# Kernel optimization log

Measured on AMD Instinct MI355X. Metric: run time of the kernel, lower is better.

## Reference

```python
import jax, jax.numpy as jnp
import numpy as np

LR = 0.01
DECAY = 0.9


def setup_inputs() -> dict:
    key = jax.random.key(0)
    ks = jax.random.split(key, 8)
    B, D_IN, H, N_FLUX, N_MET, N_IN, N_REF = 32768, 128, 1024, 512, 256, 128, 64
    return {
        "input": jax.random.normal(ks[0], (B, D_IN), jnp.float32),
        "Vref": jax.random.normal(ks[1], (B, N_REF), jnp.float32),
        "Vin": jax.random.normal(ks[2], (B, N_IN), jnp.float32),
        "W1": jax.random.normal(ks[3], (D_IN, H), jnp.float32) * 0.02,
        "b1": jnp.zeros((H,), jnp.float32),
        "W2": jax.random.normal(ks[4], (H, N_FLUX), jnp.float32) * 0.02,
        "b2": jnp.zeros((N_FLUX,), jnp.float32),
        "S": jax.random.normal(ks[5], (N_MET, N_FLUX), jnp.float32) * 0.1,
        "Pin": jax.random.normal(ks[6], (N_IN, N_FLUX), jnp.float32) * 0.1,
        "n_iteration": 30,
    }


def reference(input, Vref, Vin, W1, b1, W2, b2, S, Pin, n_iteration):
    # MLP head: Linear -> ReLU -> (Dropout inactive at eval) -> Linear
    V0 = jnp.maximum(input @ W1 + b1, 0.0) @ W2 + b2  # [B, n_flux]
    n_met = S.shape[0]
    n_in = Pin.shape[0]
    n_flux = V0.shape[1]

    def step(carry, _):
        V, diff = carry
        # dL2/dV = 2/n_met * (V S^T) S
        dV2 = (V @ S.T) @ S * (2.0 / n_met)
        # dL3/dV = 2/n_in * relu(V Pin^T - Vin) Pin  (indicator*relu == relu)
        relu_vin = jnp.maximum(V @ Pin.T - Vin, 0.0)
        dV3 = relu_vin @ Pin * (2.0 / n_in)
        # dL4/dV = -2/n_flux * relu(-V) = 2/n_flux * min(V, 0)
        dV4 = jnp.minimum(V, 0.0) * (2.0 / n_flux)
        dV = dV2 + dV3 + dV4
        diff_new = DECAY * diff - LR * dV
        return (V + diff_new, diff_new), None

    (V, _), _ = jax.lax.scan(step, (V0, jnp.zeros_like(V0)), None, length=n_iteration)
    return V
```

## Files before the change

kernel.cpp:

```cpp
#include <hip/hip_runtime.h>

typedef __bf16 bhalf;
typedef __bf16 bh8_t __attribute__((ext_vector_type(8)));
typedef float f4_t __attribute__((ext_vector_type(4)));

#define MFMA16(A, B, C) __builtin_amdgcn_mfma_f32_16x16x32_bf16((A), (B), (C), 0, 0, 0)


#define OFF_W1T  0
#define OFF_W2T  (OFF_W1T + 1024 * 128)
#define OFF_PINB (OFF_W2T + 512 * 1024)
#define OFF_PT   (OFF_PINB + 128 * 512)
#define OFF_G    (OFF_PT + 512 * 128)

__global__ __launch_bounds__(256) void amn_prep(
    const float* __restrict__ W1, const float* __restrict__ W2,
    const float* __restrict__ Pin, bhalf* __restrict__ ws) {
  unsigned i = blockIdx.x * 256u + threadIdx.x;
  if (i < 131072u) {
    unsigned n = i >> 7, k = i & 127u;
    ws[OFF_W1T + i] = (bhalf)W1[k * 1024u + n];
  } else if (i < 655360u) {
    unsigned j = i - 131072u;
    unsigned n = j >> 10, k = j & 1023u;
    ws[OFF_W2T + j] = (bhalf)W2[k * 512u + n];
  } else if (i < 720896u) {
    unsigned j = i - 655360u;
    ws[OFF_PINB + j] = (bhalf)Pin[j];
  } else if (i < 786432u) {
    unsigned j = i - 720896u;
    unsigned n = j >> 7, k = j & 127u;
    ws[OFF_PT + j] = (bhalf)(Pin[k * 512u + n] * 0.015625f);
  }
}

__global__ __launch_bounds__(256) void amn_gram(
    const float* __restrict__ S, bhalf* __restrict__ ws) {
  const unsigned bi = blockIdx.x >> 5, bj = blockIdx.x & 31u;
  __shared__ float SA[256][16];
  __shared__ float SB[256][16];
  const unsigned t = threadIdx.x;
#pragma unroll
  for (int p = 0; p < 16; ++p) {
    unsigned e = p * 256u + t;
    unsigned k = e >> 4, c = e & 15u;
    SA[k][c] = S[k * 512u + bi * 16u + c];
    SB[k][c] = S[k * 512u + bj * 16u + c];
  }
  __syncthreads();
  const unsigned ti = t >> 4, tj = t & 15u;
  float acc = 0.f;
#pragma unroll 8
  for (int k = 0; k < 256; ++k) acc += SA[k][ti] * SB[k][tj];
  ws[OFF_G + (bi * 16u + ti) * 512u + bj * 16u + tj] = (bhalf)(acc * 0.0078125f);
}

__device__ inline bh8_t cvt8(f4_t f0, f4_t f1) {
  bh8_t r;
  r[0] = (bhalf)f0[0]; r[1] = (bhalf)f0[1]; r[2] = (bhalf)f0[2]; r[3] = (bhalf)f0[3];
  r[4] = (bhalf)f1[0]; r[5] = (bhalf)f1[1]; r[6] = (bhalf)f1[2]; r[7] = (bhalf)f1[3];
  return r;
}
__device__ inline unsigned pk2(float a, float b) {
  union { bhalf h; unsigned short s; } x, y;
  x.h = (bhalf)a; y.h = (bhalf)b;
  return (unsigned)x.s | ((unsigned)y.s << 16);
}
__device__ inline float up_lo(unsigned u) {
  union { unsigned u; float f; } t; t.u = u << 16; return t.f;
}
__device__ inline float up_hi(unsigned u) {
  union { unsigned u; float f; } t; t.u = u & 0xffff0000u; return t.f;
}

__device__ inline void gload16(const void* g, void* l) {
  __builtin_amdgcn_global_load_lds(
      (const __attribute__((address_space(1))) void*)g,
      (__attribute__((address_space(3))) void*)l, 16, 0, 0);
}

#define SMBUF 33280u
#define BUFSZ 40960u
#define PREG  32768u
#define RBASE 147968u
#define SMEM_BYTES 156160

#define LGKM0   asm volatile("s_waitcnt lgkmcnt(0)" ::: "memory")
#define VMW(N)  asm volatile("s_waitcnt vmcnt(" #N ")" ::: "memory")
#define SCHEDB  __builtin_amdgcn_sched_barrier(0)
#define RAWBAR  __builtin_amdgcn_s_barrier()

#define ISSUE_GP(BO, KC) do {                                                   \
  _Pragma("unroll")                                                             \
  for (int i_ = 0; i_ < 4; ++i_) {                                              \
    unsigned s_ = w + 8u * i_;                                                  \
    gload16(Gb + gsb[i_] + (KC) * 64u, smem + SMBUF + (BO) + s_ * 1024u);       \
  }                                                                             \
  gload16(Pb + psb + (KC) * 64u, smem + SMBUF + (BO) + PREG + w * 1024u);       \
} while (0)

#define ISSUE_PT(BO, KC) do {                                                   \
  _Pragma("unroll")                                                             \
  for (int i_ = 0; i_ < 4; ++i_) {                                              \
    unsigned s_ = w + 8u * i_;                                                  \
    gload16(Ptb + ptsb[i_] + (KC) * 64u, smem + SMBUF + (BO) + s_ * 1024u);     \
  }                                                                             \
} while (0)

#define COMPUTE_GP(BO, T) do {                                                  \
  const bhalf* gb_ = (const bhalf*)(smem + SMBUF + (BO));                       \
  const bhalf* pb_ = gb_ + 16384u;                                              \
  bh8_t a0_ = *(const bh8_t*)(V_lds + lr * 520u + (T) * 32u + lq * 8u);         \
  bh8_t a1_ = *(const bh8_t*)(V_lds + (16u + lr) * 520u + (T) * 32u + lq * 8u); \
  _Pragma("unroll")                                                             \
  for (int nt_ = 0; nt_ < 4; ++nt_) {                                           \
    bh8_t bf_ = *(const bh8_t*)(gb_ + (16u * (4u * w + nt_) + lr) * 32u + lq * 8u);\
    dacc[nt_][0] = MFMA16(a0_, bf_, dacc[nt_][0]);                              \
    dacc[nt_][1] = MFMA16(a1_, bf_, dacc[nt_][1]);                              \
  }                                                                             \
  bh8_t pf_ = *(const bh8_t*)(pb_ + (16u * w + lr) * 32u + lq * 8u);            \
  Uacc[0] = MFMA16(a0_, pf_, Uacc[0]);                                          \
  Uacc[1] = MFMA16(a1_, pf_, Uacc[1]);                                          \
} while (0)

#define COMPUTE_PT(BO, C) do {                                                  \
  const bhalf* gb_ = (const bhalf*)(smem + SMBUF + (BO));                       \
  unsigned ro0_ = ((C) * 32u + lq * 8u + 8u * lr) & 127u;                       \
  bh8_t a0_ = *(const bh8_t*)(R_lds + lr * 128u + ro0_);                        \
  bh8_t a1_ = *(const bh8_t*)(R_lds + (16u + lr) * 128u + ro0_);                \
  _Pragma("unroll")                                                             \
  for (int nt_ = 0; nt_ < 4; ++nt_) {                                           \
    bh8_t bf_ = *(const bh8_t*)(gb_ + (16u * (4u * w + nt_) + lr) * 32u + lq * 8u);\
    dacc[nt_][0] = MFMA16(a0_, bf_, dacc[nt_][0]);                              \
    dacc[nt_][1] = MFMA16(a1_, bf_, dacc[nt_][1]);                              \
  }                                                                             \
} while (0)

__global__ __launch_bounds__(512) void amn_main(
    const float* __restrict__ input, const float* __restrict__ Vin,
    const float* __restrict__ b1, const float* __restrict__ b2,
    const int* __restrict__ niter_p,
    const bhalf* __restrict__ ws, float* __restrict__ out) {

  const unsigned tid = threadIdx.x;
  const unsigned w  = tid >> 6;
  const unsigned l  = tid & 63u;
  const unsigned lq = l >> 4;
  const unsigned lr = l & 15u;
  const unsigned row0 = blockIdx.x * 32u;
  const unsigned rq  = l >> 2;
  const unsigned c16 = (l & 3u) * 16u;

  const bhalf* W1t = ws + OFF_W1T;
  const bhalf* W2t = ws + OFF_W2T;
  const char* Gb  = (const char*)(ws + OFF_G);
  const char* Pb  = (const char*)(ws + OFF_PINB);
  const char* Ptb = (const char*)(ws + OFF_PT);

  __shared__ __align__(16) unsigned char smem[SMEM_BYTES];
  bhalf* hid_lds = (bhalf*)smem;
  bhalf* V_lds   = (bhalf*)smem;
  bhalf* R_lds   = (bhalf*)(smem + RBASE);

  {
    f4_t hacc[2][8];
#pragma unroll
    for (int mt = 0; mt < 2; ++mt)
#pragma unroll
      for (int t = 0; t < 8; ++t) hacc[mt][t] = (f4_t)0.f;

#pragma unroll
    for (int k = 0; k < 4; ++k) {
      bh8_t a[2];
#pragma unroll
      for (int mt = 0; mt < 2; ++mt) {
        const float* ap = input + (row0 + 16u * mt + lr) * 128u + k * 32 + lq * 8u;
        a[mt] = cvt8(*(const f4_t*)ap, *(const f4_t*)(ap + 4));
      }
#pragma unroll
      for (int t = 0; t < 8; ++t) {
        bh8_t b = *(const bh8_t*)(W1t + (16u * (8u * w + t) + lr) * 128u + k * 32 + lq * 8u);
#pragma unroll
        for (int mt = 0; mt < 2; ++mt) hacc[mt][t] = MFMA16(a[mt], b, hacc[mt][t]);
      }
    }
#pragma unroll
    for (int t = 0; t < 8; ++t) {
      unsigned col = 16u * (8u * w + t) + lr;
      float bias = b1[col];
#pragma unroll
      for (int mt = 0; mt < 2; ++mt)
#pragma unroll
        for (int r = 0; r < 4; ++r)
          hid_lds[(16u * mt + 4u * lq + r) * 1032u + col] =
              (bhalf)fmaxf(hacc[mt][t][r] + bias, 0.f);
    }
  }
  __syncthreads();

  f4_t Vreg[2][4];
#pragma unroll
  for (int mt = 0; mt < 2; ++mt)
#pragma unroll
    for (int n = 0; n < 4; ++n) Vreg[mt][n] = (f4_t)0.f;

#pragma unroll 2
  for (int k = 0; k < 32; ++k) {
    bh8_t a[2];
#pragma unroll
    for (int mt = 0; mt < 2; ++mt)
      a[mt] = *(const bh8_t*)(hid_lds + (16u * mt + lr) * 1032u + k * 32 + lq * 8u);
#pragma unroll
    for (int n = 0; n < 4; ++n) {
      bh8_t b = *(const bh8_t*)(W2t + (16u * (4u * w + n) + lr) * 1024u + k * 32 + lq * 8u);
#pragma unroll
      for (int mt = 0; mt < 2; ++mt) Vreg[mt][n] = MFMA16(a[mt], b, Vreg[mt][n]);
    }
  }
#pragma unroll
  for (int n = 0; n < 4; ++n) {
    float bias = b2[16u * (4u * w + n) + lr];
#pragma unroll
    for (int mt = 0; mt < 2; ++mt)
#pragma unroll
      for (int r = 0; r < 4; ++r) Vreg[mt][n][r] += bias;
  }

  unsigned Vinpk[2][2];
#pragma unroll
  for (int mt = 0; mt < 2; ++mt) {
    float vi[4];
#pragma unroll
    for (int r = 0; r < 4; ++r)
      vi[r] = Vin[(row0 + 16u * mt + 4u * lq + r) * 128u + 16u * w + lr];
    Vinpk[mt][0] = pk2(vi[0], vi[1]);
    Vinpk[mt][1] = pk2(vi[2], vi[3]);
  }

  unsigned Dpk[2][4][2];
#pragma unroll
  for (int mt = 0; mt < 2; ++mt)
#pragma unroll
    for (int n = 0; n < 4; ++n) { Dpk[mt][n][0] = 0u; Dpk[mt][n][1] = 0u; }

  unsigned gsb[4], ptsb[4];
#pragma unroll
  for (int j = 0; j < 4; ++j) {
    unsigned s = w + 8u * j;
    gsb[j]  = (16u * s + rq) * 1024u + c16;
    ptsb[j] = (16u * s + rq) * 256u + c16;
  }
  const unsigned psb = (16u * w + rq) * 1024u + c16;

  const int niter = niter_p[0];

  asm volatile("s_waitcnt vmcnt(0)" ::: "memory");
  __syncthreads();

  for (int it = 0; it < niter; ++it) {
#pragma unroll
    for (int mt = 0; mt < 2; ++mt)
#pragma unroll
      for (int n = 0; n < 4; ++n) {
        unsigned col = 16u * (4u * w + n) + lr;
#pragma unroll
        for (int r = 0; r < 4; ++r)
          V_lds[(16u * mt + 4u * lq + r) * 520u + col] = (bhalf)Vreg[mt][n][r];
      }
    LGKM0; SCHEDB; RAWBAR; SCHEDB;

    ISSUE_GP(0u, 0u);
    ISSUE_GP(BUFSZ, 1u);

    f4_t dacc[4][2];
#pragma unroll
    for (int nt = 0; nt < 4; ++nt) { dacc[nt][0] = (f4_t)0.f; dacc[nt][1] = (f4_t)0.f; }
    f4_t Uacc[2];
    Uacc[0] = (f4_t)0.f; Uacc[1] = (f4_t)0.f;

    unsigned cur = 0u;
#pragma unroll 1
    for (int t = 0; t < 14; ++t) {
      VMW(5); SCHEDB; RAWBAR; SCHEDB;
      COMPUTE_GP(cur, (unsigned)t);
      LGKM0; SCHEDB;
      unsigned o2 = cur + 2u * BUFSZ; if (o2 >= 3u * BUFSZ) o2 -= 3u * BUFSZ;
      ISSUE_GP(o2, (unsigned)t + 2u);
      cur += BUFSZ; if (cur >= 3u * BUFSZ) cur = 0u;
    }
    VMW(5); SCHEDB; RAWBAR; SCHEDB;
    COMPUTE_GP(2u * BUFSZ, 14u);
    LGKM0; SCHEDB;
    ISSUE_PT(BUFSZ, 0u);
    VMW(4); SCHEDB; RAWBAR; SCHEDB;
    COMPUTE_GP(0u, 15u);
#pragma unroll
    for (int mt = 0; mt < 2; ++mt) {
      float rv[4] = { fmaxf(Uacc[mt][0] - up_lo(Vinpk[mt][0]), 0.f),
                      fmaxf(Uacc[mt][1] - up_hi(Vinpk[mt][0]), 0.f),
                      fmaxf(Uacc[mt][2] - up_lo(Vinpk[mt][1]), 0.f),
                      fmaxf(Uacc[mt][3] - up_hi(Vinpk[mt][1]), 0.f) };
      unsigned col = 16u * w + lr;
#pragma unroll
      for (int r = 0; r < 4; ++r) {
        unsigned row = 16u * mt + 4u * lq + r;
        R_lds[row * 128u + ((col + 8u * row) & 127u)] = (bhalf)rv[r];
      }
    }
    LGKM0; SCHEDB;
    ISSUE_PT(2u * BUFSZ, 1u);
    VMW(4); SCHEDB; RAWBAR; SCHEDB;
    COMPUTE_PT(BUFSZ, 0u);
    LGKM0; SCHEDB;
    ISSUE_PT(0u, 2u);
    VMW(4); SCHEDB; RAWBAR; SCHEDB;
    COMPUTE_PT(2u * BUFSZ, 1u);
    LGKM0; SCHEDB;
    ISSUE_PT(BUFSZ, 3u);
    VMW(4); SCHEDB; RAWBAR; SCHEDB;
    COMPUTE_PT(0u, 2u);
    VMW(0); SCHEDB; RAWBAR; SCHEDB;
    COMPUTE_PT(BUFSZ, 3u);

#pragma unroll
    for (int nt = 0; nt < 4; ++nt)
#pragma unroll
      for (int mt = 0; mt < 2; ++mt) {
        float dv0 = dacc[nt][mt][0] + fminf(Vreg[mt][nt][0], 0.f) * 0.00390625f;
        float dv1 = dacc[nt][mt][1] + fminf(Vreg[mt][nt][1], 0.f) * 0.00390625f;
        float dv2 = dacc[nt][mt][2] + fminf(Vreg[mt][nt][2], 0.f) * 0.00390625f;
        float dv3 = dacc[nt][mt][3] + fminf(Vreg[mt][nt][3], 0.f) * 0.00390625f;
        float d0 = 0.9f * up_lo(Dpk[mt][nt][0]) - 0.01f * dv0;
        float d1 = 0.9f * up_hi(Dpk[mt][nt][0]) - 0.01f * dv1;
        float d2 = 0.9f * up_lo(Dpk[mt][nt][1]) - 0.01f * dv2;
        float d3 = 0.9f * up_hi(Dpk[mt][nt][1]) - 0.01f * dv3;
        Vreg[mt][nt][0] += d0; Vreg[mt][nt][1] += d1;
        Vreg[mt][nt][2] += d2; Vreg[mt][nt][3] += d3;
        Dpk[mt][nt][0] = pk2(d0, d1);
        Dpk[mt][nt][1] = pk2(d2, d3);
      }
  }

#pragma unroll
  for (int mt = 0; mt < 2; ++mt)
#pragma unroll
    for (int n = 0; n < 4; ++n) {
      unsigned col = 16u * (4u * w + n) + lr;
#pragma unroll
      for (int r = 0; r < 4; ++r)
        out[(row0 + 16u * mt + 4u * lq + r) * 512u + col] = Vreg[mt][n][r];
    }
}

extern "C" void kernel_launch(void* const* d_in, const int* in_sizes, int n_in,
                              void* d_out, int out_size, void* d_ws, size_t ws_size,
                              hipStream_t stream) {
  const float* input = (const float*)d_in[0];
  const float* Vin = (const float*)d_in[2];
  const float* W1  = (const float*)d_in[3];
  const float* b1  = (const float*)d_in[4];
  const float* W2  = (const float*)d_in[5];
  const float* b2  = (const float*)d_in[6];
  const float* S   = (const float*)d_in[7];
  const float* Pin = (const float*)d_in[8];
  const int* nit   = (const int*)d_in[9];
  bhalf* ws  = (bhalf*)d_ws;
  float* out = (float*)d_out;

  amn_prep<<<3072, 256, 0, stream>>>(W1, W2, Pin, ws);
  amn_gram<<<1024, 256, 0, stream>>>(S, ws);
  amn_main<<<1024, 512, 0, stream>>>(input, Vin, b1, b2, nit, ws, out);
}
```

Before: 1.695 ms.

## Make LDS staging wave-private to drop per-step barriers and deepen prefetch

```diff
diff --git a/kernel.cpp b/kernel.cpp
--- a/kernel.cpp
+++ b/kernel.cpp
@@ -92,19 +92,17 @@
 
 #define ISSUE_GP(BO, KC) do {                                                   \
   _Pragma("unroll")                                                             \
-  for (int i_ = 0; i_ < 4; ++i_) {                                              \
-    unsigned s_ = w + 8u * i_;                                                  \
-    gload16(Gb + gsb[i_] + (KC) * 64u, smem + SMBUF + (BO) + s_ * 1024u);       \
-  }                                                                             \
+  for (int i_ = 0; i_ < 4; ++i_)                                                \
+    gload16(Gb + gsb[i_] + (KC) * 64u,                                          \
+            smem + SMBUF + (BO) + (4u * w + i_) * 1024u);                       \
   gload16(Pb + psb + (KC) * 64u, smem + SMBUF + (BO) + PREG + w * 1024u);       \
 } while (0)
 
 #define ISSUE_PT(BO, KC) do {                                                   \
   _Pragma("unroll")                                                             \
-  for (int i_ = 0; i_ < 4; ++i_) {                                              \
-    unsigned s_ = w + 8u * i_;                                                  \
-    gload16(Ptb + ptsb[i_] + (KC) * 64u, smem + SMBUF + (BO) + s_ * 1024u);     \
-  }                                                                             \
+  for (int i_ = 0; i_ < 4; ++i_)                                                \
+    gload16(Ptb + ptsb[i_] + (KC) * 64u,                                        \
+            smem + SMBUF + (BO) + (4u * w + i_) * 1024u);                       \
 } while (0)
 
 #define COMPUTE_GP(BO, T) do {                                                  \
@@ -246,7 +244,7 @@
   unsigned gsb[4], ptsb[4];
 #pragma unroll
   for (int j = 0; j < 4; ++j) {
-    unsigned s = w + 8u * j;
+    unsigned s = 4u * w + j;
     gsb[j]  = (16u * s + rq) * 1024u + c16;
     ptsb[j] = (16u * s + rq) * 256u + c16;
   }
@@ -267,10 +265,11 @@
         for (int r = 0; r < 4; ++r)
           V_lds[(16u * mt + 4u * lq + r) * 520u + col] = (bhalf)Vreg[mt][n][r];
       }
-    LGKM0; SCHEDB; RAWBAR; SCHEDB;
-
+    LGKM0; SCHEDB;
     ISSUE_GP(0u, 0u);
     ISSUE_GP(BUFSZ, 1u);
+    SCHEDB; RAWBAR; SCHEDB;
+    ISSUE_GP(2u * BUFSZ, 2u);
 
     f4_t dacc[4][2];
 #pragma unroll
@@ -280,20 +279,18 @@
 
     unsigned cur = 0u;
 #pragma unroll 1
-    for (int t = 0; t < 14; ++t) {
-      VMW(5); SCHEDB; RAWBAR; SCHEDB;
+    for (int t = 0; t < 13; ++t) {
+      VMW(10); SCHEDB;
       COMPUTE_GP(cur, (unsigned)t);
       LGKM0; SCHEDB;
-      unsigned o2 = cur + 2u * BUFSZ; if (o2 >= 3u * BUFSZ) o2 -= 3u * BUFSZ;
-      ISSUE_GP(o2, (unsigned)t + 2u);
+      ISSUE_GP(cur, (unsigned)t + 3u);
       cur += BUFSZ; if (cur >= 3u * BUFSZ) cur = 0u;
     }
-    VMW(5); SCHEDB; RAWBAR; SCHEDB;
-    COMPUTE_GP(2u * BUFSZ, 14u);
-    LGKM0; SCHEDB;
-    ISSUE_PT(BUFSZ, 0u);
-    VMW(4); SCHEDB; RAWBAR; SCHEDB;
-    COMPUTE_GP(0u, 15u);
+    VMW(10); SCHEDB; COMPUTE_GP(BUFSZ, 13u); LGKM0; SCHEDB; ISSUE_PT(BUFSZ, 0u);
+    VMW(9); SCHEDB; COMPUTE_GP(2u * BUFSZ, 14u); LGKM0; SCHEDB; ISSUE_PT(2u * BUFSZ, 1u);
+    VMW(8); SCHEDB; COMPUTE_GP(0u, 15u); LGKM0; SCHEDB; ISSUE_PT(0u, 2u);
+
+    SCHEDB; RAWBAR; SCHEDB;
 #pragma unroll
     for (int mt = 0; mt < 2; ++mt) {
       float rv[4] = { fmaxf(Uacc[mt][0] - up_lo(Vinpk[mt][0]), 0.f),
@@ -307,20 +304,12 @@
         R_lds[row * 128u + ((col + 8u * row) & 127u)] = (bhalf)rv[r];
       }
     }
-    LGKM0; SCHEDB;
-    ISSUE_PT(2u * BUFSZ, 1u);
-    VMW(4); SCHEDB; RAWBAR; SCHEDB;
-    COMPUTE_PT(BUFSZ, 0u);
-    LGKM0; SCHEDB;
-    ISSUE_PT(0u, 2u);
-    VMW(4); SCHEDB; RAWBAR; SCHEDB;
-    COMPUTE_PT(2u * BUFSZ, 1u);
-    LGKM0; SCHEDB;
-    ISSUE_PT(BUFSZ, 3u);
-    VMW(4); SCHEDB; RAWBAR; SCHEDB;
-    COMPUTE_PT(0u, 2u);
-    VMW(0); SCHEDB; RAWBAR; SCHEDB;
-    COMPUTE_PT(BUFSZ, 3u);
+    LGKM0; SCHEDB; RAWBAR; SCHEDB;
+
+    VMW(8); SCHEDB; COMPUTE_PT(BUFSZ, 0u); LGKM0; SCHEDB; ISSUE_PT(BUFSZ, 3u);
+    VMW(8); SCHEDB; COMPUTE_PT(2u * BUFSZ, 1u);
+    VMW(4); SCHEDB; COMPUTE_PT(0u, 2u);
+    VMW(0); SCHEDB; COMPUTE_PT(BUFSZ, 3u);
 
 #pragma unroll
     for (int nt = 0; nt < 4; ++nt)
```

After: 1.610 ms. 5.0% less time.
